# Kernel tuning notes

Measured on AMD Instinct MI355X. Metric: run time of the kernel, lower is better.

Reference implementation:

```python
import jax, jax.numpy as jnp
import numpy as np

EPS = 1e-12  # matches torch.nn.functional.normalize default eps


def setup_inputs() -> dict:
    key = jax.random.key(0)
    k_x, k_org = jax.random.split(key)
    batch, times, d = 32, 256, 2048
    x = jax.random.normal(k_x, (batch, d, d), dtype=jnp.float32)
    # org.data.normal_(mean=0, std=0.1)
    org = 0.1 * jax.random.normal(k_org, (times, d), dtype=jnp.float32)
    return {"x": x, "org": org}


def reference(x, org):
    # F.normalize(org, dim=-1): divide each row by max(||row||_2, eps)
    norm = jnp.linalg.norm(org, axis=-1, keepdims=True)
    o = org / jnp.maximum(norm, EPS)  # (times, d)
    # Original: m = o_a (x) o_a  (rank-1 projectors, (times,d,d));
    #           y = einsum('abc,dce->dabe', m, x); trace = einsum('abcc->ab', y)
    # Algebraically: trace[batch, time] = sum_{b,c} o[a,b] * o[a,c] * x[d,c,b]
    # i.e. the quadratic form o^T x^T o per (batch, time) pair -- same math,
    # without materializing the (batch, times, d, d) intermediate.
    trace = jnp.einsum('ab,ac,dcb->da', o, o, x)  # (batch, times)
    return trace
```

## Files before the change

### kernel.cpp

```cpp
#include <hip/hip_runtime.h>
#include <hip/hip_bf16.h>

#define DDIM 2048
#define TTIMES 256
#define NT 64
#define THREADS 512

typedef __attribute__((ext_vector_type(8))) short short8;
typedef __attribute__((ext_vector_type(4))) float f32x4;

using gvoid = const __attribute__((address_space(1))) void;
using svoid = __attribute__((address_space(3))) void;

__device__ __forceinline__ void gld16(const void* g, void* l) {
    __builtin_amdgcn_global_load_lds((gvoid*)g, (svoid*)l, 16, 0, 0);
}

__device__ __forceinline__ ushort f2bf(float f) {
    union { float f; unsigned int u; } v; v.f = f;
    unsigned int u = v.u;
    unsigned int r = (u + 0x7FFFu + ((u >> 16) & 1u)) >> 16;
    return (ushort)r;
}
__device__ __forceinline__ float bf2f(ushort u) {
    union { unsigned int u; float f; } v; v.u = ((unsigned int)u) << 16;
    return v.f;
}
__device__ __forceinline__ short cvt1(float f) {
    union { __hip_bfloat16 h; ushort u; } cv;
    cv.h = __float2bfloat16(f);
    return (short)cv.u;
}

__global__ void norm_rows(const float* __restrict__ org, ushort* __restrict__ obf) {
    const int a   = blockIdx.x;
    const int tid = threadIdx.x;
    const float* row = org + (size_t)a * DDIM;
    float4 v0 = ((const float4*)row)[tid * 2];
    float4 v1 = ((const float4*)row)[tid * 2 + 1];
    float s = v0.x*v0.x + v0.y*v0.y + v0.z*v0.z + v0.w*v0.w
            + v1.x*v1.x + v1.y*v1.y + v1.z*v1.z + v1.w*v1.w;
    #pragma unroll
    for (int off = 1; off < 64; off <<= 1) s += __shfl_xor(s, off);
    __shared__ float wsum[4];
    const int lane = tid & 63, w = tid >> 6;
    if (lane == 0) wsum[w] = s;
    __syncthreads();
    const float tot = wsum[0] + wsum[1] + wsum[2] + wsum[3];
    const float scale = 1.0f / fmaxf(sqrtf(tot), 1e-12f);
    union { ushort u[8]; uint4 v; } pk;
    pk.u[0] = f2bf(v0.x * scale); pk.u[1] = f2bf(v0.y * scale);
    pk.u[2] = f2bf(v0.z * scale); pk.u[3] = f2bf(v0.w * scale);
    pk.u[4] = f2bf(v1.x * scale); pk.u[5] = f2bf(v1.y * scale);
    pk.u[6] = f2bf(v1.z * scale); pk.u[7] = f2bf(v1.w * scale);
    ((uint4*)(obf + (size_t)a * DDIM))[tid] = pk.v;
}

__global__ __launch_bounds__(THREADS, 4) void gemm_trace(
    const float* __restrict__ x, const ushort* __restrict__ obf,
    float* __restrict__ part)
{
    __shared__ __align__(16) char Ab[2][16384];
    __shared__ __align__(16) char Bb[2][16384];

    const int tid  = threadIdx.x;
    const int lane = tid & 63;
    const int wid  = tid >> 6;
    const int wm   = wid >> 2;
    const int wn   = wid & 3;
    const int rb   = blockIdx.x;
    const int d    = blockIdx.y;
    const int t0   = (d * 16 + rb) & 63;

    const char* ab = (const char*)(x + (size_t)d * DDIM * DDIM + (size_t)rb * 128 * DDIM);
    const char* bb = (const char*)obf;

    const int ar0 = tid >> 3,         aq0 = ((tid & 7) ^ (ar0 & 7)) * 16;
    const int ar1 = (tid + 512) >> 3, aq1 = (((tid + 512) & 7) ^ (ar1 & 7)) * 16;
    const int br0 = tid >> 2,         bq0 = ((tid & 3) ^ (br0 & 3)) * 16;
    const int br1 = (tid + 512) >> 2, bq1 = (((tid + 512) & 3) ^ (br1 & 3)) * 16;

    const char* as0 = ab + (size_t)ar0 * (DDIM * 4) + aq0;
    const char* as1 = ab + (size_t)ar1 * (DDIM * 4) + aq1;
    const char* bs0 = bb + (size_t)br0 * (DDIM * 2) + bq0;
    const char* bs1 = bb + (size_t)br1 * (DDIM * 2) + bq1;

#define STAGE(t, buf) do {                                \
    gld16(as0 + (t) * 128, &Ab[buf][tid * 16]);           \
    gld16(as1 + (t) * 128, &Ab[buf][(tid + 512) * 16]);   \
    gld16(bs0 + (t) * 64,  &Bb[buf][tid * 16]);           \
    gld16(bs1 + (t) * 64,  &Bb[buf][(tid + 512) * 16]);   \
} while (0)

    const int lr = lane & 15;
    const int lq = lane >> 4;

    int aoff0[4], aoff1[4], boff[4];
    #pragma unroll
    for (int mi = 0; mi < 4; ++mi) {
        const int r = wm * 64 + mi * 16 + lr;
        aoff0[mi] = r * 128 + ((2 * lq)     ^ (r & 7)) * 16;
        aoff1[mi] = r * 128 + ((2 * lq + 1) ^ (r & 7)) * 16;
    }
    #pragma unroll
    for (int ni = 0; ni < 4; ++ni) {
        const int rt = wn * 64 + ni * 16 + lr;
        boff[ni] = rt * 64 + (lq ^ (rt & 3)) * 16;
    }

    f32x4 acc[4][4];
    #pragma unroll
    for (int mi = 0; mi < 4; ++mi)
        #pragma unroll
        for (int ni = 0; ni < 4; ++ni)
            acc[mi][ni] = (f32x4){0.f, 0.f, 0.f, 0.f};

    STAGE(t0, 0);
    #pragma unroll 1
    for (int i = 0; i < NT; ++i) {
        const int cur = i & 1;
        if (i + 1 < NT) {
            STAGE(((t0 + i + 1) & 63), cur ^ 1);
            asm volatile("s_waitcnt vmcnt(4)" ::: "memory");
        } else {
            asm volatile("s_waitcnt vmcnt(0)" ::: "memory");
        }
        __builtin_amdgcn_sched_barrier(0);
        __builtin_amdgcn_s_barrier();
        __builtin_amdgcn_sched_barrier(0);

        short8 af[4], bfr[4];
        #pragma unroll
        for (int mi = 0; mi < 4; ++mi) {
            const float4 lo = *(const float4*)&Ab[cur][aoff0[mi]];
            const float4 hi = *(const float4*)&Ab[cur][aoff1[mi]];
            short8 a8;
            a8[0] = cvt1(lo.x); a8[1] = cvt1(lo.y); a8[2] = cvt1(lo.z); a8[3] = cvt1(lo.w);
            a8[4] = cvt1(hi.x); a8[5] = cvt1(hi.y); a8[6] = cvt1(hi.z); a8[7] = cvt1(hi.w);
            af[mi] = a8;
        }
        #pragma unroll
        for (int ni = 0; ni < 4; ++ni)
            bfr[ni] = *(const short8*)&Bb[cur][boff[ni]];
        #pragma unroll
        for (int mi = 0; mi < 4; ++mi)
            #pragma unroll
            for (int ni = 0; ni < 4; ++ni)
                acc[mi][ni] = __builtin_amdgcn_mfma_f32_16x16x32_bf16(
                    af[mi], bfr[ni], acc[mi][ni], 0, 0, 0);

        __builtin_amdgcn_sched_barrier(0);
        __builtin_amdgcn_s_barrier();
        __builtin_amdgcn_sched_barrier(0);
    }
#undef STAGE

    float* plds = (float*)&Ab[0][0];

    #pragma unroll
    for (int ni = 0; ni < 4; ++ni) {
        const int a_idx = wn * 64 + ni * 16 + lr;
        float ps = 0.f;
        #pragma unroll
        for (int mi = 0; mi < 4; ++mi) {
            const int bg = rb * 128 + wm * 64 + mi * 16 + lq * 4;
            const ushort4 w = *(const ushort4*)(obf + (size_t)a_idx * DDIM + bg);
            ps += bf2f(w.x) * acc[mi][ni][0];
            ps += bf2f(w.y) * acc[mi][ni][1];
            ps += bf2f(w.z) * acc[mi][ni][2];
            ps += bf2f(w.w) * acc[mi][ni][3];
        }
        ps += __shfl_xor(ps, 16);
        ps += __shfl_xor(ps, 32);
        if (lane < 16) plds[wm * 256 + a_idx] = ps;
    }
    __syncthreads();
    if (tid < 256)
        part[((size_t)d * 16 + rb) * TTIMES + tid] = plds[tid] + plds[256 + tid];
}

__global__ void reduce_part(const float* __restrict__ part, float* __restrict__ out) {
    const int d = blockIdx.x;
    const int a = threadIdx.x;
    float s = 0.f;
    #pragma unroll
    for (int rb = 0; rb < 16; ++rb)
        s += part[((size_t)d * 16 + rb) * TTIMES + a];
    out[(size_t)d * TTIMES + a] = s;
}

extern "C" void kernel_launch(void* const* d_in, const int* in_sizes, int n_in,
                              void* d_out, int out_size, void* d_ws, size_t ws_size,
                              hipStream_t stream) {
    const float* x   = (const float*)d_in[0];
    const float* org = (const float*)d_in[1];
    float* out = (float*)d_out;

    ushort* obf = (ushort*)d_ws;
    float*  prt = (float*)((char*)d_ws + (1 << 20));

    norm_rows<<<dim3(TTIMES), dim3(256), 0, stream>>>(org, obf);
    gemm_trace<<<dim3(16, 32), dim3(THREADS), 0, stream>>>(x, obf, prt);
    reduce_part<<<dim3(32), dim3(256), 0, stream>>>(prt, out);
}
```

Measured before the change: 134.4 us.

## Shrink M tile, read B directly from global, double grid for parallelism

Reduces the row tile from 128 to 64 and doubles the K step to 64, so the grid grows from 512 to 1024 blocks. The bf16 o operand is no longer staged in LDS; each lane loads its B fragments straight from global memory, which should mostly hit L2. The loop is restructured with a peeled final iteration and a waitcnt adjusted for two loads per stage. The aim is more blocks per CU and less LDS traffic, at the cost of twice as many partial sums to reduce and uncached global B loads inside the MFMA loop.

```diff
diff --git a/kernel.cpp b/kernel.cpp
--- a/kernel.cpp
+++ b/kernel.cpp
@@ -3,7 +3,9 @@
 
 #define DDIM 2048
 #define TTIMES 256
-#define NT 64
+#define BM 64
+#define BK 64
+#define NT 32
 #define THREADS 512
 
 typedef __attribute__((ext_vector_type(8))) short short8;
@@ -60,8 +62,7 @@
     const float* __restrict__ x, const ushort* __restrict__ obf,
     float* __restrict__ part)
 {
-    __shared__ __align__(16) char Ab[2][16384];
-    __shared__ __align__(16) char Bb[2][16384];
+    __shared__ __align__(16) float Ab[2][BM * BK];
 
     const int tid  = threadIdx.x;
     const int lane = tid & 63;
@@ -70,90 +71,98 @@
     const int wn   = wid & 3;
     const int rb   = blockIdx.x;
     const int d    = blockIdx.y;
-    const int t0   = (d * 16 + rb) & 63;
-
-    const char* ab = (const char*)(x + (size_t)d * DDIM * DDIM + (size_t)rb * 128 * DDIM);
-    const char* bb = (const char*)obf;
-
-    const int ar0 = tid >> 3,         aq0 = ((tid & 7) ^ (ar0 & 7)) * 16;
-    const int ar1 = (tid + 512) >> 3, aq1 = (((tid + 512) & 7) ^ (ar1 & 7)) * 16;
-    const int br0 = tid >> 2,         bq0 = ((tid & 3) ^ (br0 & 3)) * 16;
-    const int br1 = (tid + 512) >> 2, bq1 = (((tid + 512) & 3) ^ (br1 & 3)) * 16;
-
-    const char* as0 = ab + (size_t)ar0 * (DDIM * 4) + aq0;
-    const char* as1 = ab + (size_t)ar1 * (DDIM * 4) + aq1;
-    const char* bs0 = bb + (size_t)br0 * (DDIM * 2) + bq0;
-    const char* bs1 = bb + (size_t)br1 * (DDIM * 2) + bq1;
-
-#define STAGE(t, buf) do {                                \
-    gld16(as0 + (t) * 128, &Ab[buf][tid * 16]);           \
-    gld16(as1 + (t) * 128, &Ab[buf][(tid + 512) * 16]);   \
-    gld16(bs0 + (t) * 64,  &Bb[buf][tid * 16]);           \
-    gld16(bs1 + (t) * 64,  &Bb[buf][(tid + 512) * 16]);   \
+    const int t0   = (d * 32 + rb) & (NT - 1);
+
+    const char* xp = (const char*)(x + (size_t)d * DDIM * DDIM
+                                     + (size_t)rb * BM * DDIM);
+    const int v0 = wid * 128 + lane, v1 = v0 + 64;
+    const int r0 = v0 >> 4, q0 = (v0 & 15) ^ (r0 & 7);
+    const int r1 = v1 >> 4, q1 = (v1 & 15) ^ (r1 & 7);
+    const char* as0 = xp + (size_t)r0 * (DDIM * 4) + q0 * 16;
+    const char* as1 = xp + (size_t)r1 * (DDIM * 4) + q1 * 16;
+
+#define STAGE(T, buf) do {                                      \
+    gld16(as0 + (size_t)(T) * 256, (char*)Ab[buf] + v0 * 16);   \
+    gld16(as1 + (size_t)(T) * 256, (char*)Ab[buf] + v1 * 16);   \
 } while (0)
 
-    const int lr = lane & 15;
-    const int lq = lane >> 4;
-
-    int aoff0[4], aoff1[4], boff[4];
-    #pragma unroll
-    for (int mi = 0; mi < 4; ++mi) {
-        const int r = wm * 64 + mi * 16 + lr;
-        aoff0[mi] = r * 128 + ((2 * lq)     ^ (r & 7)) * 16;
-        aoff1[mi] = r * 128 + ((2 * lq + 1) ^ (r & 7)) * 16;
-    }
-    #pragma unroll
-    for (int ni = 0; ni < 4; ++ni) {
-        const int rt = wn * 64 + ni * 16 + lr;
-        boff[ni] = rt * 64 + (lq ^ (rt & 3)) * 16;
-    }
-
-    f32x4 acc[4][4];
-    #pragma unroll
-    for (int mi = 0; mi < 4; ++mi)
+    const int lr = lane & 15, lq = lane >> 4;
+    int arbase[2], arx[2];
+    #pragma unroll
+    for (int mi = 0; mi < 2; ++mi) {
+        const int r = wm * 32 + mi * 16 + lr;
+        arbase[mi] = r * BK;
+        arx[mi]    = r & 7;
+    }
+    const ushort* bt = obf + (size_t)(wn * 64 + lr) * DDIM + lq * 8;
+
+    f32x4 acc[2][4];
+    #pragma unroll
+    for (int mi = 0; mi < 2; ++mi)
         #pragma unroll
         for (int ni = 0; ni < 4; ++ni)
             acc[mi][ni] = (f32x4){0.f, 0.f, 0.f, 0.f};
 
+#define COMPUTE(cur, T) do {                                                \
+    _Pragma("unroll")                                                       \
+    for (int ss = 0; ss < 2; ++ss) {                                        \
+        short8 af[2];                                                       \
+        _Pragma("unroll")                                                   \
+        for (int mi = 0; mi < 2; ++mi) {                                    \
+            const int q = ss * 8 + lq * 2;                                  \
+            const float4 lo = *(const float4*)                              \
+                &Ab[cur][arbase[mi] + ((q)     ^ arx[mi]) * 4];             \
+            const float4 hi = *(const float4*)                              \
+                &Ab[cur][arbase[mi] + ((q + 1) ^ arx[mi]) * 4];             \
+            short8 a8;                                                      \
+            a8[0] = cvt1(lo.x); a8[1] = cvt1(lo.y);                         \
+            a8[2] = cvt1(lo.z); a8[3] = cvt1(lo.w);                         \
+            a8[4] = cvt1(hi.x); a8[5] = cvt1(hi.y);                         \
+            a8[6] = cvt1(hi.z); a8[7] = cvt1(hi.w);                         \
+            af[mi] = a8;                                                    \
+        }                                                                   \
+        short8 bb[4];                                                       \
+        _Pragma("unroll")                                                   \
+        for (int ni = 0; ni < 4; ++ni)                                      \
+            bb[ni] = *(const short8*)(bt + (size_t)ni * 16 * DDIM           \
+                                      + (T) * BK + ss * 32);                \
+        _Pragma("unroll")                                                   \
+        for (int mi = 0; mi < 2; ++mi)                                      \
+            _Pragma("unroll")                                               \
+            for (int ni = 0; ni < 4; ++ni)                                  \
+                acc[mi][ni] = __builtin_amdgcn_mfma_f32_16x16x32_bf16(      \
+                    af[mi], bb[ni], acc[mi][ni], 0, 0, 0);                  \
+    }                                                                       \
+} while (0)
+
     STAGE(t0, 0);
+
     #pragma unroll 1
-    for (int i = 0; i < NT; ++i) {
-        const int cur = i & 1;
-        if (i + 1 < NT) {
-            STAGE(((t0 + i + 1) & 63), cur ^ 1);
-            asm volatile("s_waitcnt vmcnt(4)" ::: "memory");
-        } else {
-            asm volatile("s_waitcnt vmcnt(0)" ::: "memory");
-        }
+    for (int t = 0; t < NT - 1; ++t) {
+        const int cur = t & 1;
+        const int T  = (t0 + t) & (NT - 1);
+        const int Tn = (t0 + t + 1) & (NT - 1);
+        STAGE(Tn, cur ^ 1);
+        asm volatile("s_waitcnt vmcnt(2)" ::: "memory");
         __builtin_amdgcn_sched_barrier(0);
         __builtin_amdgcn_s_barrier();
         __builtin_amdgcn_sched_barrier(0);
-
-        short8 af[4], bfr[4];
-        #pragma unroll
-        for (int mi = 0; mi < 4; ++mi) {
-            const float4 lo = *(const float4*)&Ab[cur][aoff0[mi]];
-            const float4 hi = *(const float4*)&Ab[cur][aoff1[mi]];
-            short8 a8;
-            a8[0] = cvt1(lo.x); a8[1] = cvt1(lo.y); a8[2] = cvt1(lo.z); a8[3] = cvt1(lo.w);
-            a8[4] = cvt1(hi.x); a8[5] = cvt1(hi.y); a8[6] = cvt1(hi.z); a8[7] = cvt1(hi.w);
-            af[mi] = a8;
-        }
-        #pragma unroll
-        for (int ni = 0; ni < 4; ++ni)
-            bfr[ni] = *(const short8*)&Bb[cur][boff[ni]];
-        #pragma unroll
-        for (int mi = 0; mi < 4; ++mi)
-            #pragma unroll
-            for (int ni = 0; ni < 4; ++ni)
-                acc[mi][ni] = __builtin_amdgcn_mfma_f32_16x16x32_bf16(
-                    af[mi], bfr[ni], acc[mi][ni], 0, 0, 0);
-
+        COMPUTE(cur, T);
         __builtin_amdgcn_sched_barrier(0);
         __builtin_amdgcn_s_barrier();
         __builtin_amdgcn_sched_barrier(0);
     }
+    {
+        asm volatile("s_waitcnt vmcnt(0)" ::: "memory");
+        __builtin_amdgcn_sched_barrier(0);
+        __builtin_amdgcn_s_barrier();
+        __builtin_amdgcn_sched_barrier(0);
+        COMPUTE((NT - 1) & 1, (t0 + NT - 1) & (NT - 1));
+    }
+    __syncthreads();
+
 #undef STAGE
+#undef COMPUTE
 
     float* plds = (float*)&Ab[0][0];
 
@@ -162,8 +171,8 @@
         const int a_idx = wn * 64 + ni * 16 + lr;
         float ps = 0.f;
         #pragma unroll
-        for (int mi = 0; mi < 4; ++mi) {
-            const int bg = rb * 128 + wm * 64 + mi * 16 + lq * 4;
+        for (int mi = 0; mi < 2; ++mi) {
+            const int bg = rb * BM + wm * 32 + mi * 16 + lq * 4;
             const ushort4 w = *(const ushort4*)(obf + (size_t)a_idx * DDIM + bg);
             ps += bf2f(w.x) * acc[mi][ni][0];
             ps += bf2f(w.y) * acc[mi][ni][1];
@@ -176,7 +185,7 @@
     }
     __syncthreads();
     if (tid < 256)
-        part[((size_t)d * 16 + rb) * TTIMES + tid] = plds[tid] + plds[256 + tid];
+        part[((size_t)d * 32 + rb) * TTIMES + tid] = plds[tid] + plds[256 + tid];
 }
 
 __global__ void reduce_part(const float* __restrict__ part, float* __restrict__ out) {
@@ -184,8 +193,8 @@
     const int a = threadIdx.x;
     float s = 0.f;
     #pragma unroll
-    for (int rb = 0; rb < 16; ++rb)
-        s += part[((size_t)d * 16 + rb) * TTIMES + a];
+    for (int rb = 0; rb < 32; ++rb)
+        s += part[((size_t)d * 32 + rb) * TTIMES + a];
     out[(size_t)d * TTIMES + a] = s;
 }
 
@@ -200,6 +209,6 @@
     float*  prt = (float*)((char*)d_ws + (1 << 20));
 
     norm_rows<<<dim3(TTIMES), dim3(256), 0, stream>>>(org, obf);
-    gemm_trace<<<dim3(16, 32), dim3(THREADS), 0, stream>>>(x, obf, prt);
+    gemm_trace<<<dim3(32, 32), dim3(THREADS), 0, stream>>>(x, obf, prt);
     reduce_part<<<dim3(32), dim3(256), 0, stream>>>(prt, out);
 }
```

Result: slower. 300.1 us (+123.2%).

## Triple-buffer A tiles to prefetch two k-steps ahead in gemm_trace

Applied to the files above, without the earlier changes.

Grows the fp32 x-tile LDS buffer from two to three stages and splits staging into separate A and B loads. A is now issued two iterations ahead while B stays double-buffered, and the vmcnt waits are adjusted to match. This gives more global-load latency hiding for the bandwidth-heavy fp32 x stream. In exchange LDS use rises from 64KB to 80KB per block, which may cut occupancy under the 4-blocks launch bound.

```diff
diff --git a/kernel.cpp b/kernel.cpp
--- a/kernel.cpp
+++ b/kernel.cpp
@@ -60,7 +60,7 @@
     const float* __restrict__ x, const ushort* __restrict__ obf,
     float* __restrict__ part)
 {
-    __shared__ __align__(16) char Ab[2][16384];
+    __shared__ __align__(16) char Ab[3][16384];
     __shared__ __align__(16) char Bb[2][16384];
 
     const int tid  = threadIdx.x;
@@ -70,7 +70,8 @@
     const int wn   = wid & 3;
     const int rb   = blockIdx.x;
     const int d    = blockIdx.y;
-    const int t0   = (d * 16 + rb) & 63;
+    const int t0   = (d * 16 + rb) & (NT - 1);
+#define W(n) ((t0 + (n)) & (NT - 1))
 
     const char* ab = (const char*)(x + (size_t)d * DDIM * DDIM + (size_t)rb * 128 * DDIM);
     const char* bb = (const char*)obf;
@@ -85,11 +86,13 @@
     const char* bs0 = bb + (size_t)br0 * (DDIM * 2) + bq0;
     const char* bs1 = bb + (size_t)br1 * (DDIM * 2) + bq1;
 
-#define STAGE(t, buf) do {                                \
-    gld16(as0 + (t) * 128, &Ab[buf][tid * 16]);           \
-    gld16(as1 + (t) * 128, &Ab[buf][(tid + 512) * 16]);   \
-    gld16(bs0 + (t) * 64,  &Bb[buf][tid * 16]);           \
-    gld16(bs1 + (t) * 64,  &Bb[buf][(tid + 512) * 16]);   \
+#define STAGE_A(t, buf) do {                                  \
+    gld16(as0 + (t) * 128, &Ab[buf][tid * 16]);               \
+    gld16(as1 + (t) * 128, &Ab[buf][(tid + 512) * 16]);       \
+} while (0)
+#define STAGE_B(t, buf) do {                                  \
+    gld16(bs0 + (t) * 64,  &Bb[buf][tid * 16]);               \
+    gld16(bs1 + (t) * 64,  &Bb[buf][(tid + 512) * 16]);       \
 } while (0)
 
     const int lr = lane & 15;
@@ -115,45 +118,76 @@
         for (int ni = 0; ni < 4; ++ni)
             acc[mi][ni] = (f32x4){0.f, 0.f, 0.f, 0.f};
 
-    STAGE(t0, 0);
+#define COMPUTE(abuf, bbuf) do {                                            \
+    short8 af[4], bfr[4];                                                   \
+    _Pragma("unroll")                                                       \
+    for (int mi = 0; mi < 4; ++mi) {                                        \
+        const float4 lo = *(const float4*)&Ab[abuf][aoff0[mi]];             \
+        const float4 hi = *(const float4*)&Ab[abuf][aoff1[mi]];             \
+        short8 a8;                                                          \
+        a8[0] = cvt1(lo.x); a8[1] = cvt1(lo.y);                             \
+        a8[2] = cvt1(lo.z); a8[3] = cvt1(lo.w);                             \
+        a8[4] = cvt1(hi.x); a8[5] = cvt1(hi.y);                             \
+        a8[6] = cvt1(hi.z); a8[7] = cvt1(hi.w);                             \
+        af[mi] = a8;                                                        \
+    }                                                                       \
+    _Pragma("unroll")                                                       \
+    for (int ni = 0; ni < 4; ++ni)                                          \
+        bfr[ni] = *(const short8*)&Bb[bbuf][boff[ni]];                      \
+    _Pragma("unroll")                                                       \
+    for (int mi = 0; mi < 4; ++mi)                                          \
+        _Pragma("unroll")                                                   \
+        for (int ni = 0; ni < 4; ++ni)                                      \
+            acc[mi][ni] = __builtin_amdgcn_mfma_f32_16x16x32_bf16(          \
+                af[mi], bfr[ni], acc[mi][ni], 0, 0, 0);                     \
+} while (0)
+
+#define VMW(n) do {                                                         \
+    asm volatile("s_waitcnt vmcnt(" #n ")" ::: "memory");                   \
+    __builtin_amdgcn_sched_barrier(0); } while (0)
+#define SBAR do {                                                           \
+    __builtin_amdgcn_sched_barrier(0);                                      \
+    __builtin_amdgcn_s_barrier();                                           \
+    __builtin_amdgcn_sched_barrier(0); } while (0)
+#define LGBAR do {                                                          \
+    __builtin_amdgcn_sched_barrier(0);                                      \
+    asm volatile("s_waitcnt lgkmcnt(0)" ::: "memory");                      \
+    __builtin_amdgcn_s_barrier();                                           \
+    __builtin_amdgcn_sched_barrier(0); } while (0)
+
+    STAGE_A(W(0), 0);
+    STAGE_B(W(0), 0);
+    STAGE_A(W(1), 1);
+
+    int abf = 0;
     #pragma unroll 1
-    for (int i = 0; i < NT; ++i) {
-        const int cur = i & 1;
-        if (i + 1 < NT) {
-            STAGE(((t0 + i + 1) & 63), cur ^ 1);
-            asm volatile("s_waitcnt vmcnt(4)" ::: "memory");
-        } else {
-            asm volatile("s_waitcnt vmcnt(0)" ::: "memory");
-        }
-        __builtin_amdgcn_sched_barrier(0);
-        __builtin_amdgcn_s_barrier();
-        __builtin_amdgcn_sched_barrier(0);
-
-        short8 af[4], bfr[4];
-        #pragma unroll
-        for (int mi = 0; mi < 4; ++mi) {
-            const float4 lo = *(const float4*)&Ab[cur][aoff0[mi]];
-            const float4 hi = *(const float4*)&Ab[cur][aoff1[mi]];
-            short8 a8;
-            a8[0] = cvt1(lo.x); a8[1] = cvt1(lo.y); a8[2] = cvt1(lo.z); a8[3] = cvt1(lo.w);
-            a8[4] = cvt1(hi.x); a8[5] = cvt1(hi.y); a8[6] = cvt1(hi.z); a8[7] = cvt1(hi.w);
-            af[mi] = a8;
-        }
-        #pragma unroll
-        for (int ni = 0; ni < 4; ++ni)
-            bfr[ni] = *(const short8*)&Bb[cur][boff[ni]];
-        #pragma unroll
-        for (int mi = 0; mi < 4; ++mi)
-            #pragma unroll
-            for (int ni = 0; ni < 4; ++ni)
-                acc[mi][ni] = __builtin_amdgcn_mfma_f32_16x16x32_bf16(
-                    af[mi], bfr[ni], acc[mi][ni], 0, 0, 0);
-
-        __builtin_amdgcn_sched_barrier(0);
-        __builtin_amdgcn_s_barrier();
-        __builtin_amdgcn_sched_barrier(0);
-    }
-#undef STAGE
+    for (int t = 0; t < NT - 2; ++t) {
+        STAGE_B(W(t + 1), (t + 1) & 1);
+        int ab2 = abf + 2; if (ab2 >= 3) ab2 -= 3;
+        STAGE_A(W(t + 2), ab2);
+        VMW(6);
+        SBAR;
+        COMPUTE(abf, t & 1);
+        LGBAR;
+        ++abf; if (abf == 3) abf = 0;
+    }
+    STAGE_B(W(63), 1);
+    VMW(4);
+    SBAR;
+    COMPUTE(2, 0);
+    LGBAR;
+    VMW(0);
+    SBAR;
+    COMPUTE(0, 1);
+    __syncthreads();
+
+#undef W
+#undef STAGE_A
+#undef STAGE_B
+#undef COMPUTE
+#undef VMW
+#undef SBAR
+#undef LGBAR
 
     float* plds = (float*)&Ab[0][0];
 
```

Result: no change. 133.4 us (-0.7%).
